# Kernel optimization log

Hardware: AMD Instinct MI355X
Metric: run time of the kernel (lower is better)

Reference implementation:

```python
import jax, jax.numpy as jnp
import numpy as np

EMB = 768
HEADS = 12
HD = EMB // HEADS          # 64
WS = 14                    # window size
MLP = 4 * EMB
SCALE = HD ** -0.5

# relative-position lookup indices (q_size == k_size == WS)
_REL_IDX = np.arange(WS)[:, None] - np.arange(WS)[None, :] + (WS - 1)  # (WS, WS)


def setup_inputs() -> dict:
    key = jax.random.key(0)
    ks = jax.random.split(key, 12)
    w = lambda k, shape: jax.random.normal(k, shape, jnp.float32) * 0.02
    return {
        "x": jax.random.normal(ks[0], (4, 64, 64, EMB), jnp.float32),
        "clstoken": jax.random.normal(ks[1], (4, 1, EMB), jnp.float32),
        "qkv_w": w(ks[2], (EMB, 3 * EMB)),
        "qkv_b": jnp.zeros((3 * EMB,), jnp.float32),
        "proj_w": w(ks[3], (EMB, EMB)),
        "proj_b": jnp.zeros((EMB,), jnp.float32),
        "rel_pos_h": w(ks[4], (2 * WS - 1, HD)),
        "rel_pos_w": w(ks[5], (2 * WS - 1, HD)),
        "norm1_s": jnp.ones((EMB,), jnp.float32),
        "norm1_b": jnp.zeros((EMB,), jnp.float32),
        "norm2_s": jnp.ones((EMB,), jnp.float32),
        "norm2_b": jnp.zeros((EMB,), jnp.float32),
        "fc1_w": w(ks[6], (EMB, MLP)),
        "fc1_b": jnp.zeros((MLP,), jnp.float32),
        "fc2_w": w(ks[7], (MLP, EMB)),
        "fc2_b": jnp.zeros((EMB,), jnp.float32),
    }


def _layernorm(x, s, b, eps=1e-6):
    mu = jnp.mean(x, axis=-1, keepdims=True)
    var = jnp.mean(jnp.square(x - mu), axis=-1, keepdims=True)
    return (x - mu) * jax.lax.rsqrt(var + eps) * s + b


def _attn_with_clstoken(xw, cls, qkv_w, qkv_b, proj_w, proj_b, rel_pos_h, rel_pos_w):
    # xw: (Bw, WS, WS, C), cls: (Bw, 1, C)
    Bw = xw.shape[0]
    NP = WS * WS                                   # patch tokens per window
    tokens = jnp.concatenate([cls, xw.reshape(Bw, NP, EMB)], axis=1)  # (Bw, T, C)
    T = NP + 1
    qkv = (tokens @ qkv_w + qkv_b).reshape(Bw, T, 3, HEADS, HD)
    q, k, v = [qkv[:, :, i].transpose(0, 2, 1, 3) for i in range(3)]  # (Bw, H, T, HD)
    attn = jnp.einsum("bhqd,bhkd->bhqk", q * SCALE, k)                # (Bw, H, T, T)
    # decomposed relative-position bias on the patch-patch sub-block
    Rh = rel_pos_h[_REL_IDX]                       # (WS, WS, HD)
    Rw = rel_pos_w[_REL_IDX]
    r_q = q[:, :, 1:, :].reshape(Bw, HEADS, WS, WS, HD)
    rel_h = jnp.einsum("bnhwc,hkc->bnhwk", r_q, Rh)  # (Bw, H, WS, WS, WS)
    rel_w = jnp.einsum("bnhwc,wkc->bnhwk", r_q, Rw)
    bias = (rel_h[..., :, None] + rel_w[..., None, :]).reshape(Bw, HEADS, NP, NP)
    attn = attn.at[:, :, 1:, 1:].add(bias)
    attn = jax.nn.softmax(attn, axis=-1)
    out = jnp.einsum("bhqk,bhkd->bhqd", attn, v)
    out = out.transpose(0, 2, 1, 3).reshape(Bw, T, EMB) @ proj_w + proj_b
    return out[:, 1:, :].reshape(Bw, WS, WS, EMB), out[:, :1, :]


def reference(x, clstoken, qkv_w, qkv_b, proj_w, proj_b, rel_pos_h, rel_pos_w,
              norm1_s, norm1_b, norm2_s, norm2_b, fc1_w, fc1_b, fc2_w, fc2_b):
    B, H, W, C = x.shape
    HW = H * W
    tokens = jnp.concatenate([clstoken, x.reshape(B, HW, C)], axis=1)
    shortcut = tokens
    t = _layernorm(tokens, norm1_s, norm1_b)
    cls_n = t[:, :1, :]
    xn = t[:, 1:, :].reshape(B, H, W, C)
    # window partition with padding
    pad_h = (WS - H % WS) % WS
    pad_w = (WS - W % WS) % WS
    Hp, Wp = H + pad_h, W + pad_w
    xp = jnp.pad(xn, ((0, 0), (0, pad_h), (0, pad_w), (0, 0)))
    nH, nW = Hp // WS, Wp // WS
    n_windows = nH * nW
    xw = xp.reshape(B, nH, WS, nW, WS, C).transpose(0, 1, 3, 2, 4, 5)
    xw = xw.reshape(B * n_windows, WS, WS, C)
    cls_w = jnp.repeat(cls_n, n_windows, axis=0)   # repeat_interleave over batch dim
    xw, cls_w = _attn_with_clstoken(xw, cls_w, qkv_w, qkv_b, proj_w, proj_b,
                                    rel_pos_h, rel_pos_w)
    # window unpartition
    xu = xw.reshape(B, nH, nW, WS, WS, C).transpose(0, 1, 3, 2, 4, 5)
    xu = xu.reshape(B, Hp, Wp, C)[:, :H, :W, :]
    cls_out = cls_w.reshape(B, n_windows, 1, C).mean(axis=1)
    y = jnp.concatenate([cls_out, xu.reshape(B, HW, C)], axis=1)
    tokens = shortcut + y
    h = _layernorm(tokens, norm2_s, norm2_b)
    tokens = tokens + (jax.nn.gelu(h @ fc1_w + fc1_b) @ fc2_w + fc2_b)
    return tokens  # (B, 1 + H*W, C)
```

## Files before the change

kernel.cpp:

```cpp
#include <hip/hip_runtime.h>
#include <hip/hip_bf16.h>

typedef __hip_bfloat16 bf;
typedef __bf16 bf16x8 __attribute__((ext_vector_type(8)));
typedef float f32x4 __attribute__((ext_vector_type(4)));
typedef int i32x4 __attribute__((ext_vector_type(4)));

#define DEVI __device__ __forceinline__

DEVI float b2f(bf v){ return __bfloat162float(v); }

DEVI float ldx(const void* p, size_t i, int f){
  return f ? __bfloat162float(((const bf*)p)[i]) : ((const float*)p)[i];
}

DEVI f32x4 mfma16(bf16x8 a, bf16x8 b, f32x4 c){
  return __builtin_amdgcn_mfma_f32_16x16x32_bf16(a, b, c, 0, 0, 0);
}

DEVI float gelu_t(float x){
  float u = 0.7978845608028654f * (x + 0.044715f * x * x * x);
  u = fminf(fmaxf(u, -30.f), 30.f);
  float e = __expf(2.f * u);
  return 0.5f * x * (1.f + (e - 1.f) / (e + 1.f));
}

DEVI unsigned pk2(float a, float b){
  bf x = __float2bfloat16(a), y = __float2bfloat16(b);
  unsigned short ux, uy;
  __builtin_memcpy(&ux, &x, 2); __builtin_memcpy(&uy, &y, 2);
  return (unsigned)ux | ((unsigned)uy << 16);
}

DEVI void gload16(const bf* g, char* l){
  __builtin_amdgcn_global_load_lds((const __attribute__((address_space(1))) void*)g,
                                   (__attribute__((address_space(3))) void*)l, 16, 0, 0);
}

__global__ void detect_dtype(const void* n1s, int* flag){
  unsigned u = *(const unsigned*)n1s;
  *flag = (u == 0x3F800000u) ? 0 : 1;
}

__global__ __launch_bounds__(256) void conv_bf16(const void* src, bf* dst, int n, const int* flag){
  int f = *flag;
  int i = blockIdx.x * 256 + threadIdx.x;
  if (i < n) dst[i] = f ? ((const bf*)src)[i] : __float2bfloat16(((const float*)src)[i]);
}

__global__ __launch_bounds__(256) void transpose_w(const void* __restrict__ W, bf* __restrict__ Wt,
                                                   int K, int N, const int* flag){
  __shared__ bf tile[32][33];
  const int f = *flag;
  int n0 = blockIdx.x * 32, k0 = blockIdx.y * 32;
  int tx = threadIdx.x & 31, ty = threadIdx.x >> 5;
  #pragma unroll
  for (int i = ty; i < 32; i += 8)
    tile[i][tx] = __float2bfloat16(ldx(W, (size_t)(k0 + i) * N + n0 + tx, f));
  __syncthreads();
  #pragma unroll
  for (int i = ty; i < 32; i += 8) Wt[(size_t)(n0 + i) * K + k0 + tx] = tile[tx][i];
}

DEVI void blockreduce2(float& s, float& s2){
  #pragma unroll
  for (int off = 32; off > 0; off >>= 1){
    s  += __shfl_down(s, off);
    s2 += __shfl_down(s2, off);
  }
  __shared__ float sh[8];
  int wv = threadIdx.x >> 6;
  if ((threadIdx.x & 63) == 0){ sh[wv*2] = s; sh[wv*2+1] = s2; }
  __syncthreads();
  s  = sh[0] + sh[2] + sh[4] + sh[6];
  s2 = sh[1] + sh[3] + sh[5] + sh[7];
}

__global__ __launch_bounds__(256) void ln_window(const void* __restrict__ x, const void* __restrict__ cls,
    const bf* __restrict__ g, const bf* __restrict__ bb, bf* __restrict__ winx, int b0,
    const int* flag){
  const int f = *flag;
  int row = blockIdx.x;
  int wid_g = row / 197, p = row % 197;
  int batch = b0 + wid_g / 25;
  int wid = wid_g % 25;
  int wi = wid / 5, wj = wid % 5;
  bf* dst = winx + (size_t)row * 768;
  int tid = threadIdx.x;
  const void* src = nullptr;
  size_t base = 0;
  if (p == 0){ src = cls; base = (size_t)batch * 768; }
  else {
    int pi = (p - 1) / 14, pj = (p - 1) % 14;
    int gh = wi * 14 + pi, gw = wj * 14 + pj;
    if (gh < 64 && gw < 64){ src = x; base = ((size_t)((batch * 64 + gh) * 64 + gw)) * 768; }
  }
  if (!src){
    for (int c = tid; c < 768; c += 256) dst[c] = __float2bfloat16(0.f);
    return;
  }
  float v[3]; float s = 0.f, s2 = 0.f;
  #pragma unroll
  for (int k = 0; k < 3; k++){ v[k] = ldx(src, base + tid + k*256, f); s += v[k]; s2 += v[k]*v[k]; }
  blockreduce2(s, s2);
  float mu  = s  * (1.f/768.f);
  float var = fmaxf(s2 * (1.f/768.f) - mu*mu, 0.f);
  float rs  = rsqrtf(var + 1e-6f);
  #pragma unroll
  for (int k = 0; k < 3; k++){
    int c = tid + k*256;
    dst[c] = __float2bfloat16((v[k]-mu)*rs*b2f(g[c]) + b2f(bb[c]));
  }
}

__global__ __launch_bounds__(256) void ln_f32(const float* __restrict__ in, const bf* __restrict__ g,
    const bf* __restrict__ bb, bf* __restrict__ outb){
  size_t row = blockIdx.x;
  const float* src = in + row * 768;
  bf* dst = outb + row * 768;
  int tid = threadIdx.x;
  float v[3]; float s = 0.f, s2 = 0.f;
  #pragma unroll
  for (int k = 0; k < 3; k++){ v[k] = src[tid + k*256]; s += v[k]; s2 += v[k]*v[k]; }
  blockreduce2(s, s2);
  float mu  = s  * (1.f/768.f);
  float var = fmaxf(s2 * (1.f/768.f) - mu*mu, 0.f);
  float rs  = rsqrtf(var + 1e-6f);
  #pragma unroll
  for (int k = 0; k < 3; k++){
    int c = tid + k*256;
    dst[c] = __float2bfloat16((v[k]-mu)*rs*b2f(g[c]) + b2f(bb[c]));
  }
}

__global__ __launch_bounds__(512) void gemm128(const bf* __restrict__ A, const bf* __restrict__ Bt,
    const bf* __restrict__ bias, const float* __restrict__ res, void* __restrict__ out,
    int M, int N, int K, int flags, const int* dflag, int row_off)
{
  __shared__ __bf16 sA[2][128*64];
  __shared__ __bf16 sB[2][128*64];
  const int df = *dflag;
  const int gx = gridDim.x;
  const int nwg = gx * gridDim.y;
  const int lin = blockIdx.y * gx + blockIdx.x;
  const int q = nwg >> 3, r = nwg & 7;
  const int xcd = lin & 7, pos = lin >> 3;
  const int logical = (xcd < r ? xcd * (q + 1) : r * (q + 1) + (xcd - r) * q) + pos;
  const int m0 = (logical / gx) * 128, n0 = (logical % gx) * 128;

  const int tid = threadIdx.x, wv = tid >> 6, l = tid & 63;
  const int wm = (wv >> 2) * 64;
  const int wn = (wv & 3) * 32;
  const int li = l & 15, lk = l >> 4;
  const int xr = li & 7;

  f32x4 acc[4][2];
  #pragma unroll
  for (int i = 0; i < 4; i++)
    #pragma unroll
    for (int j = 0; j < 2; j++){ f32x4 z = {0.f,0.f,0.f,0.f}; acc[i][j] = z; }

  const int rA = tid >> 3;
  const int sl = (tid & 7) ^ (rA & 7);
  const bf* gA0 = A  + (size_t)(m0 + rA)      * K + sl * 8;
  const bf* gA1 = A  + (size_t)(m0 + 64 + rA) * K + sl * 8;
  const bf* gB0 = Bt + (size_t)(n0 + rA)      * K + sl * 8;
  const bf* gB1 = Bt + (size_t)(n0 + 64 + rA) * K + sl * 8;
  const int ldsbase = wv * 1024;

  const int nt = K >> 6;
  {
    gload16(gA0, (char*)sA[0] + ldsbase);
    gload16(gA1, (char*)sA[0] + 8192 + ldsbase);
    gload16(gB0, (char*)sB[0] + ldsbase);
    gload16(gB1, (char*)sB[0] + 8192 + ldsbase);
  }
  asm volatile("s_waitcnt vmcnt(0)" ::: "memory");
  __syncthreads();

  int cur = 0;
  for (int t = 0; t < nt; t++){
    if (t + 1 < nt){
      const int ke = (t + 1) << 6;
      gload16(gA0 + ke, (char*)sA[cur^1] + ldsbase);
      gload16(gA1 + ke, (char*)sA[cur^1] + 8192 + ldsbase);
      gload16(gB0 + ke, (char*)sB[cur^1] + ldsbase);
      gload16(gB1 + ke, (char*)sB[cur^1] + 8192 + ldsbase);
    }
    const __bf16* cA = sA[cur];
    const __bf16* cB = sB[cur];
    #pragma unroll
    for (int ks = 0; ks < 2; ks++){
      const int so = ((ks*4 + lk) ^ xr) * 8;
      bf16x8 af[4], bfr[2];
      #pragma unroll
      for (int i = 0; i < 4; i++) af[i]  = *(const bf16x8*)&cA[(wm + i*16 + li)*64 + so];
      #pragma unroll
      for (int j = 0; j < 2; j++) bfr[j] = *(const bf16x8*)&cB[(wn + j*16 + li)*64 + so];
      #pragma unroll
      for (int i = 0; i < 4; i++)
        #pragma unroll
        for (int j = 0; j < 2; j++) acc[i][j] = mfma16(af[i], bfr[j], acc[i][j]);
    }
    asm volatile("s_waitcnt vmcnt(0)" ::: "memory");
    __syncthreads();
    cur ^= 1;
  }

  #pragma unroll
  for (int i = 0; i < 4; i++){
    #pragma unroll
    for (int j = 0; j < 2; j++){
      int colg = n0 + wn + j*16 + li;
      float bc = b2f(bias[colg]);
      #pragma unroll
      for (int r2 = 0; r2 < 4; r2++){
        int rowg = m0 + wm + i*16 + lk*4 + r2;
        if (rowg < M){
          float vv = acc[i][j][r2] + bc;
          if (flags & 1) vv = gelu_t(vv);
          if (flags & 2) vv += res[(size_t)rowg * N + colg];
          if (flags & 4){
            size_t oidx = (size_t)(row_off + rowg) * N + colg;
            if (df == 0) ((float*)out)[oidx] = vv;
            else         ((bf*)out)[oidx]    = __float2bfloat16(vv);
          } else {
            ((bf*)out)[(size_t)rowg * N + colg] = __float2bfloat16(vv);
          }
        }
      }
    }
  }
}

__global__ __launch_bounds__(256) void bias_tables(const bf* __restrict__ qkv,
    const bf* __restrict__ rph, const bf* __restrict__ rpw, bf* __restrict__ relT){
  const int blk = blockIdx.x;
  const int w = blk / 12, h = blk % 12;
  const int tid = threadIdx.x, wv = tid >> 6, l = tid & 63;
  const int li = l & 15, lk = l >> 4;
  const bf* qbase = qkv + (size_t)w * 197 * 2304 + h * 64;
  bf* tbase = relT + (size_t)blk * 7056;
  for (int g = wv; g < 28; g += 4){
    bool isH = (g < 14);
    int pfix = isH ? g : (g - 14);
    int var  = li < 13 ? li : 13;
    int q = isH ? (1 + pfix*14 + var) : (1 + var*14 + pfix);
    f32x4 acc = {0.f,0.f,0.f,0.f};
    const bf* rp = isH ? rph : rpw;
    #pragma unroll
    for (int s = 0; s < 2; s++){
      bf16x8 a = *(const bf16x8*)(qbase + (size_t)q * 2304 + s*32 + lk*8);
      int idx = pfix + 13 - li;
      if (idx < 0) idx = 0;
      bf16x8 b = *(const bf16x8*)(rp + idx * 64 + s*32 + lk*8);
      acc = mfma16(a, b, acc);
    }
    #pragma unroll
    for (int r = 0; r < 4; r++){
      int mrow = lk*4 + r;
      int col = li;
      if (mrow <= 13 && col <= 13){
        int qi = isH ? (pfix*14 + mrow) : (mrow*14 + pfix);
        tbase[(isH ? 0 : 3528) + qi*18 + col] = __float2bfloat16(acc[r]);
      }
    }
  }
}

__global__ __launch_bounds__(256) void attn_win(const bf* __restrict__ qkv,
    const bf* __restrict__ relT, bf* __restrict__ aout){
  __shared__ __bf16 VtL[64*232];
  __shared__ __bf16 relL[8192];
  const int blk = blockIdx.x;
  const int wh = blk >> 1, half = blk & 1;
  const int w = wh / 12, h = wh % 12;
  const int tid = threadIdx.x, wv = tid >> 6, l = tid & 63;
  const int li = l & 15, lk = l >> 4;
  const bf* qp = qkv + (size_t)wh / 12 * 0 + (size_t)w * 197 * 2304 + h * 64;
  const bf* kp = qp + 768;
  const bf* vp = qp + 1536;

  {
    const bf* tbase = relT + (size_t)wh * 7056;
    #pragma unroll
    for (int p = 0; p < 4; p++)
      gload16(tbase + p*2048 + (size_t)tid * 8, (char*)relL + p*4096 + wv * 1024);
  }
  {
    const int cc = (tid & 7) * 8, rb = tid >> 3;
    const int xw = (tid & 7) << 3;
    #pragma unroll
    for (int pass = 0; pass < 7; pass++){
      int r = pass * 32 + rb;
      __bf16 vvv[8];
      if (r < 197){
        bf16x8 t = *(const bf16x8*)(vp + (size_t)r * 2304 + cc);
        #pragma unroll
        for (int e = 0; e < 8; e++) vvv[e] = t[e];
      } else {
        #pragma unroll
        for (int e = 0; e < 8; e++) vvv[e] = (__bf16)0.f;
      }
      #pragma unroll
      for (int e = 0; e < 8; e++)
        VtL[(((cc + e) * 232 + r) ^ xw)] = vvv[e];
    }
  }
  asm volatile("s_waitcnt vmcnt(0)" ::: "memory");
  __syncthreads();

  const int qt0 = half * 7;
  const int nqt = half ? 6 : 7;
  for (int qt_l = wv; qt_l < nqt; qt_l += 4){
    const int qt = qt0 + qt_l;
    const int myq = qt * 16 + li;
    int qrow = myq > 196 ? 196 : myq;
    bf16x8 qa0 = *(const bf16x8*)(qp + (size_t)qrow * 2304 + lk*8);
    bf16x8 qa1 = *(const bf16x8*)(qp + (size_t)qrow * 2304 + 32 + lk*8);
    f32x4 sc[13];
    #pragma unroll
    for (int ct = 0; ct < 13; ct++){
      int kr = ct * 16 + li; if (kr > 196) kr = 196;
      bf16x8 kb0 = *(const bf16x8*)(kp + (size_t)kr * 2304 + lk*8);
      bf16x8 kb1 = *(const bf16x8*)(kp + (size_t)kr * 2304 + 32 + lk*8);
      f32x4 z = {0.f,0.f,0.f,0.f};
      z = mfma16(kb0, qa0, z);
      z = mfma16(kb1, qa1, z);
      sc[ct] = z;
    }
    const bool qok = (myq >= 1 && myq < 197);
    const int qi18 = (myq - 1) * 18;
    float mx = -3e38f;
    #pragma unroll
    for (int ct = 0; ct < 13; ct++){
      #pragma unroll
      for (int r = 0; r < 4; r++){
        int key = ct*16 + lk*4 + r;
        float s = sc[ct][r] * 0.125f;
        if (key >= 197) s = -1e30f;
        else if (key >= 1 && qok){
          int ki = key - 1;
          int kh = (ki * 4682) >> 16;
          int kw = ki - kh * 14;
          s += b2f(*(const bf*)&relL[qi18 + kh]) + b2f(*(const bf*)&relL[3528 + qi18 + kw]);
        }
        sc[ct][r] = s;
        mx = fmaxf(mx, s);
      }
    }
    mx = fmaxf(mx, __shfl_xor(mx, 16));
    mx = fmaxf(mx, __shfl_xor(mx, 32));
    float den = 0.f;
    #pragma unroll
    for (int ct = 0; ct < 13; ct++)
      #pragma unroll
      for (int r = 0; r < 4; r++){
        float e = __expf(sc[ct][r] - mx);
        sc[ct][r] = e; den += e;
      }
    den += __shfl_xor(den, 16);
    den += __shfl_xor(den, 32);
    float rden = 1.f / den;
    unsigned pw0[13], pw1[13];
    #pragma unroll
    for (int ct = 0; ct < 13; ct++){
      pw0[ct] = pk2(sc[ct][0]*rden, sc[ct][1]*rden);
      pw1[ct] = pk2(sc[ct][2]*rden, sc[ct][3]*rden);
    }
    const int selhi = (lk >> 1) & 1;
    const int srcA = li + ((lk & 1) << 5);
    const int srcB = srcA + 16;
    f32x4 o[4];
    #pragma unroll
    for (int n = 0; n < 4; n++){ f32x4 z = {0.f,0.f,0.f,0.f}; o[n] = z; }
    #pragma unroll
    for (int wn32 = 0; wn32 < 7; wn32++){
      const int t0 = 2*wn32, t1 = 2*wn32 + 1;
      unsigned s0a = __shfl(pw0[t0], srcA);
      unsigned s1a = __shfl(pw1[t0], srcA);
      unsigned s0b = __shfl(pw0[t0], srcB);
      unsigned s1b = __shfl(pw1[t0], srcB);
      unsigned u0a = 0, u1a = 0, u0b = 0, u1b = 0;
      if (t1 < 13){
        u0a = __shfl(pw0[t1], srcA);
        u1a = __shfl(pw1[t1], srcA);
        u0b = __shfl(pw0[t1], srcB);
        u1b = __shfl(pw1[t1], srcB);
      }
      i32x4 aw;
      aw[0] = (int)(selhi ? u0a : s0a);
      aw[1] = (int)(selhi ? u1a : s1a);
      aw[2] = (int)(selhi ? u0b : s0b);
      aw[3] = (int)(selhi ? u1b : s1b);
      bf16x8 af = *(bf16x8*)&aw;
      #pragma unroll
      for (int n = 0; n < 4; n++){
        int dim = n*16 + li;
        int bidx = (dim*232 + wn32*32 + lk*8) ^ (((dim >> 3) & 7) << 3);
        bf16x8 vb = *(const bf16x8*)&VtL[bidx];
        o[n] = mfma16(af, vb, o[n]);
      }
    }
    #pragma unroll
    for (int n = 0; n < 4; n++){
      #pragma unroll
      for (int r = 0; r < 4; r++){
        int grow = qt*16 + lk*4 + r;
        if (grow < 197)
          aout[((size_t)w * 197 + grow) * 768 + h*64 + n*16 + li] = __float2bfloat16(o[n][r]);
      }
    }
  }
}

__global__ __launch_bounds__(256) void unwindow(const void* __restrict__ x, const void* __restrict__ cls,
    const bf* __restrict__ projoC, float* __restrict__ tok2, int b0, const int* flag){
  const int f = *flag;
  int tg = blockIdx.x;
  int bl = tg / 4097, t = tg % 4097;
  int batch = b0 + bl;
  const bf* projo = projoC + (size_t)bl * 4925 * 768;
  for (int c = threadIdx.x; c < 768; c += 256){
    float val, add;
    if (t == 0){
      val = ldx(cls, (size_t)batch * 768 + c, f);
      float s = 0.f;
      #pragma unroll
      for (int wi = 0; wi < 25; wi++)
        s += b2f(projo[((size_t)wi * 197) * 768 + c]);
      add = s * 0.04f;
    } else {
      int idx = t - 1, gh = idx >> 6, gw = idx & 63;
      int wi = gh / 14, pi = gh % 14, wj = gw / 14, pj = gw % 14;
      int wwin = wi*5 + wj, tl = 1 + pi*14 + pj;
      val = ldx(x, ((size_t)batch * 4096 + idx) * 768 + c, f);
      add = b2f(projo[((size_t)wwin * 197 + tl) * 768 + c]);
    }
    tok2[((size_t)batch * 4097 + t) * 768 + c] = val + add;
  }
}

extern "C" void kernel_launch(void* const* d_in, const int* in_sizes, int n_in,
                              void* d_out, int out_size, void* d_ws, size_t ws_size,
                              hipStream_t stream){
  (void)in_sizes; (void)n_in; (void)out_size;
  const void* x      = d_in[0];
  const void* cls    = d_in[1];
  const void* qkv_w  = d_in[2];
  const void* qkv_bv = d_in[3];
  const void* proj_w = d_in[4];
  const void* proj_bv= d_in[5];
  const void* rph    = d_in[6];
  const void* rpw    = d_in[7];
  const void* n1s    = d_in[8];
  const void* n1b    = d_in[9];
  const void* n2s    = d_in[10];
  const void* n2b    = d_in[11];
  const void* fc1_w  = d_in[12];
  const void* fc1_bv = d_in[13];
  const void* fc2_w  = d_in[14];
  const void* fc2_bv = d_in[15];

  char* ws = (char*)d_ws;
  int* flagp  = (int*)(ws + 0);
  bf* wt_qkv  = (bf*)(ws + 256);
  bf* wt_proj = (bf*)(ws + 3539200);
  bf* wt_fc1  = (bf*)(ws + 4718848);
  bf* wt_fc2  = (bf*)(ws + 9437440);
  bf* c_qkv_b = (bf*)(ws + 14156032);
  bf* c_proj_b= (bf*)(ws + 14160640);
  bf* c_fc1_b = (bf*)(ws + 14162176);
  bf* c_fc2_b = (bf*)(ws + 14168320);
  bf* c_n1s   = (bf*)(ws + 14169856);
  bf* c_n1b   = (bf*)(ws + 14171392);
  bf* c_n2s   = (bf*)(ws + 14172928);
  bf* c_n2b   = (bf*)(ws + 14174464);
  bf* c_rph   = (bf*)(ws + 14176000);
  bf* c_rpw   = (bf*)(ws + 14179456);

  const size_t base0 = 14188800;
  int nb = 1;
  if      (ws_size >= base0 + 4ull*37824000 + 50343936) nb = 4;
  else if (ws_size >= base0 + 2ull*37824000 + 50343936) nb = 2;
  const size_t o_winx  = base0;
  const size_t o_qkv   = o_winx + (size_t)nb * 7564800;
  const size_t o_projo = o_qkv  + (size_t)nb * 22694400;
  const size_t o_tok2  = o_projo+ (size_t)nb * 7564800;
  const size_t o_fc1g  = base0  + (size_t)nb * 6292992;

  bf* winx_c  = (bf*)(ws + o_winx);
  bf* attn_oC = winx_c;
  bf* qkvC    = (bf*)(ws + o_qkv);
  bf* projoC  = (bf*)(ws + o_projo);
  bf* relT    = (bf*)(ws + o_projo);
  float* tok2 = (float*)(ws + o_tok2);
  bf* hbufC   = (bf*)(ws + base0);
  bf* fc1gC   = (bf*)(ws + o_fc1g);

  detect_dtype<<<1, 1, 0, stream>>>(n1s, flagp);

  conv_bf16<<<9,  256, 0, stream>>>(qkv_bv,  c_qkv_b, 2304, flagp);
  conv_bf16<<<3,  256, 0, stream>>>(proj_bv, c_proj_b, 768, flagp);
  conv_bf16<<<12, 256, 0, stream>>>(fc1_bv,  c_fc1_b, 3072, flagp);
  conv_bf16<<<3,  256, 0, stream>>>(fc2_bv,  c_fc2_b,  768, flagp);
  conv_bf16<<<3,  256, 0, stream>>>(n1s, c_n1s, 768, flagp);
  conv_bf16<<<3,  256, 0, stream>>>(n1b, c_n1b, 768, flagp);
  conv_bf16<<<3,  256, 0, stream>>>(n2s, c_n2s, 768, flagp);
  conv_bf16<<<3,  256, 0, stream>>>(n2b, c_n2b, 768, flagp);
  conv_bf16<<<7,  256, 0, stream>>>(rph, c_rph, 1728, flagp);
  conv_bf16<<<7,  256, 0, stream>>>(rpw, c_rpw, 1728, flagp);

  transpose_w<<<dim3(72, 24), 256, 0, stream>>>(qkv_w, wt_qkv, 768, 2304, flagp);
  transpose_w<<<dim3(24, 24), 256, 0, stream>>>(proj_w, wt_proj, 768, 768, flagp);
  transpose_w<<<dim3(96, 24), 256, 0, stream>>>(fc1_w, wt_fc1, 768, 3072, flagp);
  transpose_w<<<dim3(24, 96), 256, 0, stream>>>(fc2_w, wt_fc2, 3072, 768, flagp);

  const int nchunk = 4 / nb;
  for (int ci = 0; ci < nchunk; ci++){
    const int b0 = ci * nb;
    const int Mq = nb * 4925;
    const int gy = (Mq + 127) / 128;
    ln_window<<<nb*4925, 256, 0, stream>>>(x, cls, c_n1s, c_n1b, winx_c, b0, flagp);
    gemm128<<<dim3(18, gy), 512, 0, stream>>>(winx_c, wt_qkv, c_qkv_b, nullptr, qkvC,
                                              Mq, 2304, 768, 0, flagp, 0);
    bias_tables<<<nb*300, 256, 0, stream>>>(qkvC, c_rph, c_rpw, relT);
    attn_win<<<nb*600, 256, 0, stream>>>(qkvC, relT, attn_oC);
    gemm128<<<dim3(6, gy), 512, 0, stream>>>(attn_oC, wt_proj, c_proj_b, nullptr, projoC,
                                             Mq, 768, 768, 0, flagp, 0);
    unwindow<<<nb*4097, 256, 0, stream>>>(x, cls, projoC, tok2, b0, flagp);
  }

  for (int ci = 0; ci < nchunk; ci++){
    const int b0 = ci * nb;
    const int Mm = nb * 4097;
    const int gym = (Mm + 127) / 128;
    ln_f32<<<Mm, 256, 0, stream>>>(tok2 + (size_t)b0 * 4097 * 768, c_n2s, c_n2b, hbufC);
    gemm128<<<dim3(24, gym), 512, 0, stream>>>(hbufC, wt_fc1, c_fc1_b, nullptr, fc1gC,
                                               Mm, 3072, 768, 1, flagp, 0);
    gemm128<<<dim3(6, gym), 512, 0, stream>>>(fc1gC, wt_fc2, c_fc2_b,
                                              tok2 + (size_t)b0 * 4097 * 768,
                                              d_out,
                                              Mm, 768, 3072, 2 | 4, flagp, b0 * 4097);
  }
}
```

Baseline: 666.1 us.

## Fuse bias tables into attention, stage K in LDS, fuse LN2 into unwindow

The relative-position bias table computation moves inside the attention kernel and writes straight to shared memory, which removes a separate launch and a global round trip. K rows are staged once into swizzled LDS instead of being re-read from global memory per query tile. Blocks are remapped across XCDs for locality. When all batches fit in one chunk, the second layernorm is fused into the unwindow kernel, which skips the ln_f32 pass. The cost is more LDS per block, which may lower occupancy, and each half-block pair now recomputes the bias tables.

```diff
diff --git a/kernel.cpp b/kernel.cpp
--- a/kernel.cpp
+++ b/kernel.cpp
@@ -9,6 +9,12 @@
 #define DEVI __device__ __forceinline__
 
 DEVI float b2f(bf v){ return __bfloat162float(v); }
+
+DEVI __bf16 f2h(float v){
+  bf t = __float2bfloat16(v);
+  __bf16 h; __builtin_memcpy(&h, &t, 2);
+  return h;
+}
 
 DEVI float ldx(const void* p, size_t i, int f){
   return f ? __bfloat162float(((const bf*)p)[i]) : ((const float*)p)[i];
@@ -233,59 +239,48 @@
   }
 }
 
-__global__ __launch_bounds__(256) void bias_tables(const bf* __restrict__ qkv,
-    const bf* __restrict__ rph, const bf* __restrict__ rpw, bf* __restrict__ relT){
-  const int blk = blockIdx.x;
-  const int w = blk / 12, h = blk % 12;
+__global__ __launch_bounds__(256) void attn_win(const bf* __restrict__ qkv,
+    const bf* __restrict__ rph, const bf* __restrict__ rpw, bf* __restrict__ aout){
+  __shared__ __bf16 VtL[64*232];
+  __shared__ __bf16 relL[7056];
+  __shared__ __bf16 KL[208*64];
+  const int nwg = gridDim.x;
+  const int lin = blockIdx.x;
+  const int q8 = nwg >> 3, r8 = nwg & 7;
+  const int xcd = lin & 7, pos = lin >> 3;
+  const int blk = (xcd < r8 ? xcd * (q8 + 1) : r8 * (q8 + 1) + (xcd - r8) * q8) + pos;
+  const int wh = blk >> 1, half = blk & 1;
+  const int w = wh / 12, h = wh % 12;
   const int tid = threadIdx.x, wv = tid >> 6, l = tid & 63;
   const int li = l & 15, lk = l >> 4;
-  const bf* qbase = qkv + (size_t)w * 197 * 2304 + h * 64;
-  bf* tbase = relT + (size_t)blk * 7056;
+  const bf* qp = qkv + (size_t)w * 197 * 2304 + h * 64;
+  const bf* kp = qp + 768;
+  const bf* vp = qp + 1536;
+
   for (int g = wv; g < 28; g += 4){
     bool isH = (g < 14);
     int pfix = isH ? g : (g - 14);
     int var  = li < 13 ? li : 13;
-    int q = isH ? (1 + pfix*14 + var) : (1 + var*14 + pfix);
+    int qq = isH ? (1 + pfix*14 + var) : (1 + var*14 + pfix);
     f32x4 acc = {0.f,0.f,0.f,0.f};
     const bf* rp = isH ? rph : rpw;
     #pragma unroll
     for (int s = 0; s < 2; s++){
-      bf16x8 a = *(const bf16x8*)(qbase + (size_t)q * 2304 + s*32 + lk*8);
+      bf16x8 a = *(const bf16x8*)(qp + (size_t)qq * 2304 + s*32 + lk*8);
       int idx = pfix + 13 - li;
       if (idx < 0) idx = 0;
       bf16x8 b = *(const bf16x8*)(rp + idx * 64 + s*32 + lk*8);
       acc = mfma16(a, b, acc);
     }
     #pragma unroll
-    for (int r = 0; r < 4; r++){
-      int mrow = lk*4 + r;
+    for (int r_ = 0; r_ < 4; r_++){
+      int mrow = lk*4 + r_;
       int col = li;
       if (mrow <= 13 && col <= 13){
         int qi = isH ? (pfix*14 + mrow) : (mrow*14 + pfix);
-        tbase[(isH ? 0 : 3528) + qi*18 + col] = __float2bfloat16(acc[r]);
-      }
-    }
-  }
-}
-
-__global__ __launch_bounds__(256) void attn_win(const bf* __restrict__ qkv,
-    const bf* __restrict__ relT, bf* __restrict__ aout){
-  __shared__ __bf16 VtL[64*232];
-  __shared__ __bf16 relL[8192];
-  const int blk = blockIdx.x;
-  const int wh = blk >> 1, half = blk & 1;
-  const int w = wh / 12, h = wh % 12;
-  const int tid = threadIdx.x, wv = tid >> 6, l = tid & 63;
-  const int li = l & 15, lk = l >> 4;
-  const bf* qp = qkv + (size_t)wh / 12 * 0 + (size_t)w * 197 * 2304 + h * 64;
-  const bf* kp = qp + 768;
-  const bf* vp = qp + 1536;
-
-  {
-    const bf* tbase = relT + (size_t)wh * 7056;
-    #pragma unroll
-    for (int p = 0; p < 4; p++)
-      gload16(tbase + p*2048 + (size_t)tid * 8, (char*)relL + p*4096 + wv * 1024);
+        relL[(isH ? 0 : 3528) + qi*18 + col] = f2h(acc[r_]);
+      }
+    }
   }
   {
     const int cc = (tid & 7) * 8, rb = tid >> 3;
@@ -307,11 +302,28 @@
         VtL[(((cc + e) * 232 + r) ^ xw)] = vvv[e];
     }
   }
-  asm volatile("s_waitcnt vmcnt(0)" ::: "memory");
+  {
+    const int slot = tid & 7, rb = tid >> 3;
+    #pragma unroll
+    for (int pass = 0; pass < 7; pass++){
+      int r = pass * 32 + rb;
+      if (r < 208){
+        bf16x8 t;
+        if (r < 197){
+          t = *(const bf16x8*)(kp + (size_t)r * 2304 + slot*8);
+        } else {
+          #pragma unroll
+          for (int e = 0; e < 8; e++) t[e] = (__bf16)0.f;
+        }
+        *(bf16x8*)&KL[r*64 + ((slot ^ (r & 7)))*8] = t;
+      }
+    }
+  }
   __syncthreads();
 
   const int qt0 = half * 7;
   const int nqt = half ? 6 : 7;
+  const int xrk = li & 7;
   for (int qt_l = wv; qt_l < nqt; qt_l += 4){
     const int qt = qt0 + qt_l;
     const int myq = qt * 16 + li;
@@ -321,9 +333,9 @@
     f32x4 sc[13];
     #pragma unroll
     for (int ct = 0; ct < 13; ct++){
-      int kr = ct * 16 + li; if (kr > 196) kr = 196;
-      bf16x8 kb0 = *(const bf16x8*)(kp + (size_t)kr * 2304 + lk*8);
-      bf16x8 kb1 = *(const bf16x8*)(kp + (size_t)kr * 2304 + 32 + lk*8);
+      int kr = ct * 16 + li;
+      bf16x8 kb0 = *(const bf16x8*)&KL[kr*64 + ((lk    ) ^ xrk)*8];
+      bf16x8 kb1 = *(const bf16x8*)&KL[kr*64 + ((lk + 4) ^ xrk)*8];
       f32x4 z = {0.f,0.f,0.f,0.f};
       z = mfma16(kb0, qa0, z);
       z = mfma16(kb1, qa1, z);
@@ -414,14 +426,19 @@
   }
 }
 
-__global__ __launch_bounds__(256) void unwindow(const void* __restrict__ x, const void* __restrict__ cls,
-    const bf* __restrict__ projoC, float* __restrict__ tok2, int b0, const int* flag){
+__global__ __launch_bounds__(256) void unwin_ln(const void* __restrict__ x, const void* __restrict__ cls,
+    const bf* __restrict__ projoC, float* __restrict__ tok2, bf* __restrict__ hbuf,
+    const bf* __restrict__ g, const bf* __restrict__ bb, int b0, const int* flag, int doLN){
   const int f = *flag;
   int tg = blockIdx.x;
   int bl = tg / 4097, t = tg % 4097;
   int batch = b0 + bl;
   const bf* projo = projoC + (size_t)bl * 4925 * 768;
-  for (int c = threadIdx.x; c < 768; c += 256){
+  int tid = threadIdx.x;
+  float v[3];
+  #pragma unroll
+  for (int k = 0; k < 3; k++){
+    int c = tid + k*256;
     float val, add;
     if (t == 0){
       val = ldx(cls, (size_t)batch * 768 + c, f);
@@ -437,7 +454,20 @@
       val = ldx(x, ((size_t)batch * 4096 + idx) * 768 + c, f);
       add = b2f(projo[((size_t)wwin * 197 + tl) * 768 + c]);
     }
-    tok2[((size_t)batch * 4097 + t) * 768 + c] = val + add;
+    v[k] = val + add;
+    tok2[((size_t)batch * 4097 + t) * 768 + c] = v[k];
+  }
+  if (!doLN) return;
+  float s = v[0]+v[1]+v[2], s2 = v[0]*v[0]+v[1]*v[1]+v[2]*v[2];
+  blockreduce2(s, s2);
+  float mu  = s  * (1.f/768.f);
+  float var = fmaxf(s2 * (1.f/768.f) - mu*mu, 0.f);
+  float rs  = rsqrtf(var + 1e-6f);
+  bf* dst = hbuf + ((size_t)bl * 4097 + t) * 768;
+  #pragma unroll
+  for (int k = 0; k < 3; k++){
+    int c = tid + k*256;
+    dst[c] = __float2bfloat16((v[k]-mu)*rs*b2f(g[c]) + b2f(bb[c]));
   }
 }
 
@@ -493,7 +523,6 @@
   bf* attn_oC = winx_c;
   bf* qkvC    = (bf*)(ws + o_qkv);
   bf* projoC  = (bf*)(ws + o_projo);
-  bf* relT    = (bf*)(ws + o_projo);
   float* tok2 = (float*)(ws + o_tok2);
   bf* hbufC   = (bf*)(ws + base0);
   bf* fc1gC   = (bf*)(ws + o_fc1g);
@@ -517,6 +546,7 @@
   transpose_w<<<dim3(24, 96), 256, 0, stream>>>(fc2_w, wt_fc2, 3072, 768, flagp);
 
   const int nchunk = 4 / nb;
+  const int doLN = (nchunk == 1) ? 1 : 0;
   for (int ci = 0; ci < nchunk; ci++){
     const int b0 = ci * nb;
     const int Mq = nb * 4925;
@@ -524,18 +554,19 @@
     ln_window<<<nb*4925, 256, 0, stream>>>(x, cls, c_n1s, c_n1b, winx_c, b0, flagp);
     gemm128<<<dim3(18, gy), 512, 0, stream>>>(winx_c, wt_qkv, c_qkv_b, nullptr, qkvC,
                                               Mq, 2304, 768, 0, flagp, 0);
-    bias_tables<<<nb*300, 256, 0, stream>>>(qkvC, c_rph, c_rpw, relT);
-    attn_win<<<nb*600, 256, 0, stream>>>(qkvC, relT, attn_oC);
+    attn_win<<<nb*600, 256, 0, stream>>>(qkvC, c_rph, c_rpw, attn_oC);
     gemm128<<<dim3(6, gy), 512, 0, stream>>>(attn_oC, wt_proj, c_proj_b, nullptr, projoC,
                                              Mq, 768, 768, 0, flagp, 0);
-    unwindow<<<nb*4097, 256, 0, stream>>>(x, cls, projoC, tok2, b0, flagp);
+    unwin_ln<<<nb*4097, 256, 0, stream>>>(x, cls, projoC, tok2, hbufC,
+                                          c_n2s, c_n2b, b0, flagp, doLN);
   }
 
   for (int ci = 0; ci < nchunk; ci++){
     const int b0 = ci * nb;
     const int Mm = nb * 4097;
     const int gym = (Mm + 127) / 128;
-    ln_f32<<<Mm, 256, 0, stream>>>(tok2 + (size_t)b0 * 4097 * 768, c_n2s, c_n2b, hbufC);
+    if (!doLN)
+      ln_f32<<<Mm, 256, 0, stream>>>(tok2 + (size_t)b0 * 4097 * 768, c_n2s, c_n2b, hbufC);
     gemm128<<<dim3(24, gym), 512, 0, stream>>>(hbufC, wt_fc1, c_fc1_b, nullptr, fc1gC,
                                                Mm, 3072, 768, 1, flagp, 0);
     gemm128<<<dim3(6, gym), 512, 0, stream>>>(fc1gC, wt_fc2, c_fc2_b,
```

Result: no change. 679.4 us (+2.0%).
